# Kernel optimization log

Measured on AMD Instinct MI355X. Metric: run time of the kernel, lower is better.

The kernel has to match this reference:

```python
import jax, jax.numpy as jnp
import numpy as np

LN_EPS = 1e-5
ROPE_BASE = 10000.0


def rotate_half(x):
    # x: [..., d]; split into two halves (matches einops '(j d)->j d', j=2)
    d2 = x.shape[-1] // 2
    x1, x2 = x[..., :d2], x[..., d2:]
    return jnp.concatenate((-x2, x1), axis=-1)


def rotary_pos_emb(n, head_dim, dtype=jnp.float32):
    inv_freq = 1.0 / (ROPE_BASE ** (jnp.arange(0, head_dim, 2, dtype=jnp.float32) / head_dim))
    t = jnp.arange(n, dtype=jnp.float32)
    freqs = jnp.einsum('i,j->ij', t, inv_freq)          # [n, d/2]
    return jnp.concatenate((freqs, freqs), axis=-1).astype(dtype)  # [n, d]


def apply_rotary(pos, t):
    return t * jnp.cos(pos) + rotate_half(t) * jnp.sin(pos)


def setup_inputs() -> dict:
    key = jax.random.key(0)
    ks = jax.random.split(key, 4)
    b, n, dm = 2, 4096, 2048
    x = jax.random.normal(ks[0], (b, n, dm), dtype=jnp.float32)
    wq = jax.random.normal(ks[1], (dm, dm), dtype=jnp.float32) * (dm ** -0.5)
    wk = jax.random.normal(ks[2], (dm, dm), dtype=jnp.float32) * (dm ** -0.5)
    wv = jax.random.normal(ks[3], (dm, dm), dtype=jnp.float32) * (dm ** -0.5)
    return {
        'x': x,
        'ln_gamma': jnp.ones((dm,), jnp.float32),
        'ln_beta': jnp.zeros((dm,), jnp.float32),
        'wq': wq, 'wk': wk, 'wv': wv,
        'num_heads': 16,
    }


def reference(x, ln_gamma, ln_beta, wq, wk, wv, num_heads):
    b, n, dm = x.shape
    hd = dm // num_heads
    # LayerNorm (eps=1e-5, torch default)
    mu = jnp.mean(x, axis=-1, keepdims=True)
    var = jnp.mean(jnp.square(x - mu), axis=-1, keepdims=True)
    xn = (x - mu) * jax.lax.rsqrt(var + LN_EPS) * ln_gamma + ln_beta
    # QKV projections (nn.Linear, bias=False => x @ W.T; weights stored as [out,in])
    q = jnp.einsum('bnd,ed->bne', xn, wq)
    k = jnp.einsum('bnd,ed->bne', xn, wk)
    v = jnp.einsum('bnd,ed->bne', xn, wv)
    # b n (h d) -> b h n d
    split = lambda t: t.reshape(b, n, num_heads, hd).transpose(0, 2, 1, 3)
    q, k, v = split(q), split(k), split(v)
    pos = rotary_pos_emb(n, hd, x.dtype)  # [n, hd], broadcasts over b,h
    q = apply_rotary(pos, q)
    k = apply_rotary(pos, k)
    return q, k, v
```

## Files before the change

kernel.cpp:

```cpp
#include <hip/hip_runtime.h>
#include <hip/hip_bf16.h>


typedef float f32x4 __attribute__((ext_vector_type(4)));
typedef __bf16 bf16x8 __attribute__((ext_vector_type(8)));
typedef __bf16 bf16x4 __attribute__((ext_vector_type(4)));

#define DM    2048
#define NSEQ  4096
#define NH    16
#define HD    128
#define NROWS 8192
#define MAT_ELEMS (2ull*NH*NSEQ*HD)

typedef __attribute__((address_space(1))) const void GV;
typedef __attribute__((address_space(3))) void LV;
__device__ __forceinline__ void gload_lds16(const void* g, void* l) {
    __builtin_amdgcn_global_load_lds((GV*)g, (LV*)l, 16, 0, 0);
}

__global__ __launch_bounds__(256)
void ln_kernel(const float* __restrict__ x, const float* __restrict__ g,
               const float* __restrict__ be, __bf16* __restrict__ xnb) {
    int row = blockIdx.x;
    int tid = threadIdx.x;
    const float4* xr = (const float4*)(x + (size_t)row * DM);
    float4 v0 = xr[tid];
    float4 v1 = xr[tid + 256];
    float s  = v0.x + v0.y + v0.z + v0.w + v1.x + v1.y + v1.z + v1.w;
    float ss = v0.x*v0.x + v0.y*v0.y + v0.z*v0.z + v0.w*v0.w
             + v1.x*v1.x + v1.y*v1.y + v1.z*v1.z + v1.w*v1.w;
#pragma unroll
    for (int o = 32; o > 0; o >>= 1) {
        s  += __shfl_down(s, o);
        ss += __shfl_down(ss, o);
    }
    __shared__ float red[10];
    int wave = tid >> 6, lane = tid & 63;
    if (lane == 0) { red[wave] = s; red[4 + wave] = ss; }
    __syncthreads();
    if (tid == 0) {
        float S  = red[0] + red[1] + red[2] + red[3];
        float SS = red[4] + red[5] + red[6] + red[7];
        float mu  = S * (1.0f / DM);
        float var = SS * (1.0f / DM) - mu * mu;
        red[8] = mu;
        red[9] = rsqrtf(var + 1e-5f);
    }
    __syncthreads();
    float mu = red[8], rs = red[9];

    const float4* gp = (const float4*)g;
    const float4* bp = (const float4*)be;
    bf16x4* orow = (bf16x4*)(xnb + (size_t)row * DM);
    {
        float4 g0 = gp[tid], b0 = bp[tid];
        bf16x4 o;
        o[0] = (__bf16)((v0.x - mu) * rs * g0.x + b0.x);
        o[1] = (__bf16)((v0.y - mu) * rs * g0.y + b0.y);
        o[2] = (__bf16)((v0.z - mu) * rs * g0.z + b0.z);
        o[3] = (__bf16)((v0.w - mu) * rs * g0.w + b0.w);
        orow[tid] = o;
    }
    {
        float4 g1 = gp[tid + 256], b1 = bp[tid + 256];
        bf16x4 o;
        o[0] = (__bf16)((v1.x - mu) * rs * g1.x + b1.x);
        o[1] = (__bf16)((v1.y - mu) * rs * g1.y + b1.y);
        o[2] = (__bf16)((v1.z - mu) * rs * g1.z + b1.z);
        o[3] = (__bf16)((v1.w - mu) * rs * g1.w + b1.w);
        orow[tid + 256] = o;
    }
}

__global__ __launch_bounds__(256)
void cvt3_kernel(const float* __restrict__ a0, const float* __restrict__ a1,
                 const float* __restrict__ a2, __bf16* __restrict__ o) {
    int bid = blockIdx.x;
    const float* a = (bid < 2048) ? a0 : (bid < 4096) ? a1 : a2;
    size_t base = ((size_t)(bid & 2047) * 256 + threadIdx.x) * 8;
    float4 v0 = *(const float4*)(a + base);
    float4 v1 = *(const float4*)(a + base + 4);
    bf16x8 r;
    r[0] = (__bf16)v0.x; r[1] = (__bf16)v0.y; r[2] = (__bf16)v0.z; r[3] = (__bf16)v0.w;
    r[4] = (__bf16)v1.x; r[5] = (__bf16)v1.y; r[6] = (__bf16)v1.z; r[7] = (__bf16)v1.w;
    *(bf16x8*)(o + (size_t)(bid >> 11) * 4194304 + base) = r;
}


__device__ __forceinline__ void loadA4(bf16x8 (&a)[4][2], const __bf16* Sp,
                                       int base, int mb, int o0) {
#pragma unroll
    for (int mi = 0; mi < 4; mi++)
#pragma unroll
        for (int ks = 0; ks < 2; ks++)
            a[mi][ks] = *(const bf16x8*)(Sp + base + (mb + mi) * 1024 + (o0 ^ (ks * 32)));
}
__device__ __forceinline__ void loadB2(bf16x8 (&b)[2][2], const __bf16* Sp,
                                       int base, int cb, int o0) {
#pragma unroll
    for (int f = 0; f < 2; f++)
#pragma unroll
        for (int ks = 0; ks < 2; ks++)
            b[f][ks] = *(const bf16x8*)(Sp + base + (f * 16 + (cb >> 1) * 64) * 64 + (o0 ^ (ks * 32)));
}

template<int RB, int CB>
__device__ __forceinline__ void cluster(f32x4 (&acc)[8][4], bf16x8 (&a)[4][2],
                                        bf16x8 (&b)[2][2]) {
    __builtin_amdgcn_s_setprio(1);
#pragma unroll
    for (int mi = 0; mi < 4; mi++)
#pragma unroll
        for (int ni = 0; ni < 2; ni++)
#pragma unroll
            for (int ks = 0; ks < 2; ks++)
                acc[RB + mi][CB + ni] = __builtin_amdgcn_mfma_f32_16x16x32_bf16(
                    a[mi][ks], b[ni][ks], acc[RB + mi][CB + ni], 0, 0, 0);
    __builtin_amdgcn_s_setprio(0);
}

#define FENCE asm volatile("" ::: "memory")
#define BAR   do { FENCE; __builtin_amdgcn_s_barrier(); FENCE; } while (0)
#define VM8   asm volatile("s_waitcnt vmcnt(8)" ::: "memory")
#define VM4   asm volatile("s_waitcnt vmcnt(4)" ::: "memory")
#define VM2   asm volatile("s_waitcnt vmcnt(2)" ::: "memory")
#define VM0   asm volatile("s_waitcnt vmcnt(0)" ::: "memory")
#define VMX   do {} while (0)

#define STGA(P, kt, HF) do { \
    gload_lds16(pA + (size_t)((HF) * 64 + w * 8) * DM + (kt) * 64,       &As[P][((HF) * 8 + w) * 512]); \
    gload_lds16(pA + (size_t)((HF) * 64 + 128 + w * 8) * DM + (kt) * 64, &As[P][((HF) * 8 + 16 + w) * 512]); \
} while (0)
#define STGB(P, kt, HF) do { \
    gload_lds16(pB + (size_t)((HF) * 64 + w * 8) * DM + (kt) * 64,       &Bs[P][((HF) * 8 + w) * 512]); \
    gload_lds16(pB + (size_t)((HF) * 64 + 128 + w * 8) * DM + (kt) * 64, &Bs[P][((HF) * 8 + 16 + w) * 512]); \
} while (0)

#define KTILE(kt, P, Q, SG0, SG1, SG2, SG3, W0, W1, W2, W3) do { \
     \
    loadA4(a,  &As[P][0], baseA, 0, o0); \
    loadB2(b0, &Bs[P][0], baseB, 0, o0); \
    if (SG0) STGA(Q, (kt) + 1, 1);                \
    W0; BAR; cluster<0, 0>(acc, a, b0); BAR; \
     \
    loadB2(b1, &Bs[P][0], baseB, 2, o0); \
    if (SG1) STGA(P, (kt) + 2, 0);                \
    W1; BAR; cluster<0, 2>(acc, a, b1); BAR; \
     \
    loadA4(a, &As[P][0], baseA, 4, o0); \
    if (SG2) STGB(P, (kt) + 2, 0);                \
    W2; BAR; cluster<4, 2>(acc, a, b1); BAR; \
     \
    if (SG3) STGB(P, (kt) + 2, 1);                \
    W3; BAR; cluster<4, 0>(acc, a, b0); BAR; \
} while (0)

__global__ __launch_bounds__(512, 2)
void gemm_qkv(const __bf16* __restrict__ A,
              const __bf16* __restrict__ Wq,
              const __bf16* __restrict__ Wk,
              const __bf16* __restrict__ Wv,
              float* __restrict__ out) {
    __shared__ __bf16 As[2][16384];
    __shared__ __bf16 Bs[2][16384];

    int tid = threadIdx.x;
    int w = tid >> 6, l = tid & 63;
    int wm = w >> 2, wn = w & 3;

    int bid = blockIdx.x;
    int x = bid & 7;
    int ridx = bid >> 3;
    int q = ridx >> 5;
    int s = ridx & 31;
    int mtp, ntp;
    if (q == 0)      { mtp = s >> 3;       ntp = s & 7; }
    else if (q == 1) { mtp = 4 + (s >> 3); ntp = s & 7; }
    else             { mtp = s & 7;        ntp = 8 + (s >> 3); }
    int mt = (x & 3) * 8 + mtp;
    int nt = (x >> 2) * 12 + ntp;
    int mat = nt >> 3, ntb = nt & 7;
    const __bf16* Wp = (mat == 0) ? Wq : (mat == 1) ? Wk : Wv;
    int row0 = mt * 256, colp = ntb * 256;

    int lr = l >> 3;
    int lco = ((l & 7) ^ lr) * 8;
    const __bf16* pA = A  + (size_t)(row0 + lr) * DM + lco;
    const __bf16* pB = Wp + (size_t)(colp + lr) * DM + lco;

    int baseA = (wm * 128 + (l & 15)) * 64;
    int baseB = ((wn & 1) * 32 + (wn >> 1) * 128 + (l & 15)) * 64;
    int o0 = ((l >> 4) * 8) ^ ((l & 7) * 8);

    STGA(0, 0, 0); STGA(0, 0, 1); STGB(0, 0, 0); STGB(0, 0, 1);
    STGA(1, 1, 0); STGB(1, 1, 0); STGB(1, 1, 1);

    f32x4 acc[8][4];
#pragma unroll
    for (int i = 0; i < 8; i++)
#pragma unroll
        for (int j = 0; j < 4; j++)
            acc[i][j] = (f32x4){0.f, 0.f, 0.f, 0.f};

    bf16x8 a[4][2], b0[2][2], b1[2][2];

    VM8;
    BAR;

#pragma unroll 1
    for (int kt = 0; kt < 30; kt += 2) {
        KTILE(kt,     0, 1, 1, 1, 1, 1, VM8, VM8, VMX, VM8);
        KTILE(kt + 1, 1, 0, 1, 1, 1, 1, VM8, VM8, VMX, VM8);
    }
    KTILE(30, 0, 1, 1, 0, 0, 0, VM8, VM8, VMX, VM4);
    KTILE(31, 1, 0, 0, 0, 0, 0, VM2, VM0, VMX, VMX);

    float* op = out + (size_t)mat * MAT_ELEMS;
    int hd_lo = (wn & 1) * 32 + (l & 15);
    int head = ntb * 2 + (wn >> 1);
    int r_base = row0 + wm * 128 + ((l >> 4) << 2);
    float if0 = exp2f(-0.20762051f * (float)hd_lo);
    float if1 = exp2f(-0.20762051f * (float)(hd_lo + 16));

    if (mat < 2) {
#pragma unroll
        for (int mi = 0; mi < 8; mi++) {
#pragma unroll
            for (int j = 0; j < 4; j++) {
                int r = r_base + mi * 16 + j;
                int b = r >> 12, n = r & 4095;
                float fn = (float)n;
                float* rowp = op + ((size_t)((b * NH + head) * NSEQ + n)) * HD;
#pragma unroll
                for (int ni = 0; ni < 2; ni++) {
                    float lo = acc[mi][ni][j], hi = acc[mi][ni + 2][j];
                    float sv, cv;
                    __sincosf(fn * (ni ? if1 : if0), &sv, &cv);
                    rowp[hd_lo + ni * 16]      = lo * cv - hi * sv;
                    rowp[hd_lo + ni * 16 + 64] = hi * cv + lo * sv;
                }
            }
        }
    } else {
#pragma unroll
        for (int mi = 0; mi < 8; mi++) {
#pragma unroll
            for (int j = 0; j < 4; j++) {
                int r = r_base + mi * 16 + j;
                int b = r >> 12, n = r & 4095;
                float* rowp = op + ((size_t)((b * NH + head) * NSEQ + n)) * HD;
#pragma unroll
                for (int ni = 0; ni < 2; ni++) {
                    rowp[hd_lo + ni * 16]      = acc[mi][ni][j];
                    rowp[hd_lo + ni * 16 + 64] = acc[mi][ni + 2][j];
                }
            }
        }
    }
}

extern "C" void kernel_launch(void* const* d_in, const int* in_sizes, int n_in,
                              void* d_out, int out_size, void* d_ws, size_t ws_size,
                              hipStream_t stream) {
    const float* x  = (const float*)d_in[0];
    const float* g  = (const float*)d_in[1];
    const float* be = (const float*)d_in[2];
    const float* wq = (const float*)d_in[3];
    const float* wk = (const float*)d_in[4];
    const float* wv = (const float*)d_in[5];
    float* out = (float*)d_out;

    char* ws = (char*)d_ws;
    __bf16* xnb = (__bf16*)ws;
    __bf16* wb  = (__bf16*)(ws + 33554432);

    ln_kernel<<<NROWS, 256, 0, stream>>>(x, g, be, xnb);
    cvt3_kernel<<<6144, 256, 0, stream>>>(wq, wk, wv, wb);
    gemm_qkv<<<768, 512, 0, stream>>>(xnb, wb, wb + 4194304, wb + 8388608, out);
}
```

Measured before the change: 225.3 us.

## Restructure GEMM k-tile into k-split phases with full N fragments per cluster

Each 64-wide k-tile is now split into two 32-wide k halves. Each compute phase loads four A and four B fragments for one k half and issues 16 MFMAs over the full 4-column output, where before each phase covered two columns and both k halves. The global-to-LDS staging is regrouped so the A and B half-tiles for kt+2 are issued together, and the vmcnt wait points and the prologue load order change to match. The aim is to cut LDS fragment reloads (B is read once per k half instead of twice per tile) and rebalance memory waits, at the cost of more live fragment registers and a different overlap of loads with MFMA work.

```diff
diff --git a/kernel.cpp b/kernel.cpp
--- a/kernel.cpp
+++ b/kernel.cpp
@@ -88,42 +88,36 @@
 }
 
 
-__device__ __forceinline__ void loadA4(bf16x8 (&a)[4][2], const __bf16* Sp,
-                                       int base, int mb, int o0) {
+__device__ __forceinline__ void loadA(bf16x8 (&a)[4], const __bf16* Sp,
+                                      int base, int oo) {
 #pragma unroll
     for (int mi = 0; mi < 4; mi++)
-#pragma unroll
-        for (int ks = 0; ks < 2; ks++)
-            a[mi][ks] = *(const bf16x8*)(Sp + base + (mb + mi) * 1024 + (o0 ^ (ks * 32)));
-}
-__device__ __forceinline__ void loadB2(bf16x8 (&b)[2][2], const __bf16* Sp,
-                                       int base, int cb, int o0) {
-#pragma unroll
-    for (int f = 0; f < 2; f++)
-#pragma unroll
-        for (int ks = 0; ks < 2; ks++)
-            b[f][ks] = *(const bf16x8*)(Sp + base + (f * 16 + (cb >> 1) * 64) * 64 + (o0 ^ (ks * 32)));
-}
-
-template<int RB, int CB>
-__device__ __forceinline__ void cluster(f32x4 (&acc)[8][4], bf16x8 (&a)[4][2],
-                                        bf16x8 (&b)[2][2]) {
+        a[mi] = *(const bf16x8*)(Sp + base + mi * 1024 + oo);
+}
+__device__ __forceinline__ void loadB(bf16x8 (&b)[4], const __bf16* Sp,
+                                      int base, int oo) {
+#pragma unroll
+    for (int j = 0; j < 4; j++)
+        b[j] = *(const bf16x8*)(Sp + base + (j * 16 + (j >> 1) * 32) * 64 + oo);
+}
+
+template<int RB>
+__device__ __forceinline__ void cluster(f32x4 (&acc)[8][4], bf16x8 (&a)[4],
+                                        bf16x8 (&b)[4]) {
     __builtin_amdgcn_s_setprio(1);
 #pragma unroll
     for (int mi = 0; mi < 4; mi++)
 #pragma unroll
-        for (int ni = 0; ni < 2; ni++)
-#pragma unroll
-            for (int ks = 0; ks < 2; ks++)
-                acc[RB + mi][CB + ni] = __builtin_amdgcn_mfma_f32_16x16x32_bf16(
-                    a[mi][ks], b[ni][ks], acc[RB + mi][CB + ni], 0, 0, 0);
+        for (int ni = 0; ni < 4; ni++)
+            acc[RB + mi][ni] = __builtin_amdgcn_mfma_f32_16x16x32_bf16(
+                a[mi], b[ni], acc[RB + mi][ni], 0, 0, 0);
     __builtin_amdgcn_s_setprio(0);
 }
 
 #define FENCE asm volatile("" ::: "memory")
 #define BAR   do { FENCE; __builtin_amdgcn_s_barrier(); FENCE; } while (0)
 #define VM8   asm volatile("s_waitcnt vmcnt(8)" ::: "memory")
-#define VM4   asm volatile("s_waitcnt vmcnt(4)" ::: "memory")
+#define VM6   asm volatile("s_waitcnt vmcnt(6)" ::: "memory")
 #define VM2   asm volatile("s_waitcnt vmcnt(2)" ::: "memory")
 #define VM0   asm volatile("s_waitcnt vmcnt(0)" ::: "memory")
 #define VMX   do {} while (0)
@@ -137,23 +131,24 @@
     gload_lds16(pB + (size_t)((HF) * 64 + 128 + w * 8) * DM + (kt) * 64, &Bs[P][((HF) * 8 + 16 + w) * 512]); \
 } while (0)
 
-#define KTILE(kt, P, Q, SG0, SG1, SG2, SG3, W0, W1, W2, W3) do { \
-     \
-    loadA4(a,  &As[P][0], baseA, 0, o0); \
-    loadB2(b0, &Bs[P][0], baseB, 0, o0); \
-    if (SG0) STGA(Q, (kt) + 1, 1);                \
-    W0; BAR; cluster<0, 0>(acc, a, b0); BAR; \
-     \
-    loadB2(b1, &Bs[P][0], baseB, 2, o0); \
-    if (SG1) STGA(P, (kt) + 2, 0);                \
-    W1; BAR; cluster<0, 2>(acc, a, b1); BAR; \
-     \
-    loadA4(a, &As[P][0], baseA, 4, o0); \
-    if (SG2) STGB(P, (kt) + 2, 0);                \
-    W2; BAR; cluster<4, 2>(acc, a, b1); BAR; \
-     \
-    if (SG3) STGB(P, (kt) + 2, 1);                \
-    W3; BAR; cluster<4, 0>(acc, a, b0); BAR; \
+#define KTILE(kt, P, Q, SG0, SG2, SG3, W0, W2) do { \
+     \
+    loadA(a0, &As[P][0], baseA, o0); \
+    loadB(b0, &Bs[P][0], baseB, o0); \
+    if (SG0) STGA(Q, (kt) + 1, 1); \
+    W0; BAR; cluster<0>(acc, a0, b0); BAR; \
+     \
+    loadA(a1, &As[P][0], baseA, o1); \
+    loadB(b1, &Bs[P][0], baseB, o1); \
+    BAR; cluster<0>(acc, a1, b1); BAR; \
+     \
+    loadA(a0, &As[P][0], baseA + 4096, o0); \
+    if (SG2) { STGA(P, (kt) + 2, 0); STGB(P, (kt) + 2, 0); } \
+    W2; BAR; cluster<4>(acc, a0, b0); BAR; \
+     \
+    loadA(a1, &As[P][0], baseA + 4096, o1); \
+    if (SG3) STGB(P, (kt) + 2, 1); \
+    BAR; cluster<4>(acc, a1, b1); BAR; \
 } while (0)
 
 __global__ __launch_bounds__(512, 2)
@@ -192,8 +187,9 @@
     int baseA = (wm * 128 + (l & 15)) * 64;
     int baseB = ((wn & 1) * 32 + (wn >> 1) * 128 + (l & 15)) * 64;
     int o0 = ((l >> 4) * 8) ^ ((l & 7) * 8);
-
-    STGA(0, 0, 0); STGA(0, 0, 1); STGB(0, 0, 0); STGB(0, 0, 1);
+    int o1 = o0 ^ 32;
+
+    STGA(0, 0, 0); STGB(0, 0, 0); STGB(0, 0, 1); STGA(0, 0, 1);
     STGA(1, 1, 0); STGB(1, 1, 0); STGB(1, 1, 1);
 
     f32x4 acc[8][4];
@@ -203,18 +199,18 @@
         for (int j = 0; j < 4; j++)
             acc[i][j] = (f32x4){0.f, 0.f, 0.f, 0.f};
 
-    bf16x8 a[4][2], b0[2][2], b1[2][2];
+    bf16x8 a0[4], a1[4], b0[4], b1[4];
 
     VM8;
     BAR;
 
 #pragma unroll 1
     for (int kt = 0; kt < 30; kt += 2) {
-        KTILE(kt,     0, 1, 1, 1, 1, 1, VM8, VM8, VMX, VM8);
-        KTILE(kt + 1, 1, 0, 1, 1, 1, 1, VM8, VM8, VMX, VM8);
-    }
-    KTILE(30, 0, 1, 1, 0, 0, 0, VM8, VM8, VMX, VM4);
-    KTILE(31, 1, 0, 0, 0, 0, 0, VM2, VM0, VMX, VMX);
+        KTILE(kt,     0, 1, 1, 1, 1, VM8, VM6);
+        KTILE(kt + 1, 1, 0, 1, 1, 1, VM8, VM6);
+    }
+    KTILE(30, 0, 1, 1, 0, 0, VM8, VM2);
+    KTILE(31, 1, 0, 0, 0, 0, VM0, VMX);
 
     float* op = out + (size_t)mat * MAT_ELEMS;
     int hd_lo = (wn & 1) * 32 + (l & 15);
```

After: 233.8 us. 1.04x slower.

## Fuse LayerNorm and weight conversion launches; restructure GEMM vmcnt/lgkm waits

Applied to the files above, without the earlier changes.

Merges the LayerNorm and fp32-to-bf16 weight conversion kernels into one launch that branches on block index, removing one kernel launch and its tail. In the GEMM main loop the per-stage vmcnt waits are replaced by a single vmcnt(6) wait per k-tile plus an explicit lgkmcnt(0) wait and scheduling barrier after each barrier. The prologue load order is also changed to match. This may cut wait stalls but risks serializing LDS reads before the MFMA clusters.

```diff
diff --git a/kernel.cpp b/kernel.cpp
--- a/kernel.cpp
+++ b/kernel.cpp
@@ -20,71 +20,73 @@
 }
 
 __global__ __launch_bounds__(256)
-void ln_kernel(const float* __restrict__ x, const float* __restrict__ g,
-               const float* __restrict__ be, __bf16* __restrict__ xnb) {
-    int row = blockIdx.x;
+void lncvt_kernel(const float* __restrict__ x, const float* __restrict__ g,
+                  const float* __restrict__ be,
+                  const float* __restrict__ wq, const float* __restrict__ wk,
+                  const float* __restrict__ wv,
+                  __bf16* __restrict__ xnb, __bf16* __restrict__ wb) {
+    int bid = blockIdx.x;
     int tid = threadIdx.x;
-    const float4* xr = (const float4*)(x + (size_t)row * DM);
-    float4 v0 = xr[tid];
-    float4 v1 = xr[tid + 256];
-    float s  = v0.x + v0.y + v0.z + v0.w + v1.x + v1.y + v1.z + v1.w;
-    float ss = v0.x*v0.x + v0.y*v0.y + v0.z*v0.z + v0.w*v0.w
-             + v1.x*v1.x + v1.y*v1.y + v1.z*v1.z + v1.w*v1.w;
-#pragma unroll
-    for (int o = 32; o > 0; o >>= 1) {
-        s  += __shfl_down(s, o);
-        ss += __shfl_down(ss, o);
+    if (bid < NROWS) {
+        int row = bid;
+        const float4* xr = (const float4*)(x + (size_t)row * DM);
+        float4 v0 = xr[tid];
+        float4 v1 = xr[tid + 256];
+        float s  = v0.x + v0.y + v0.z + v0.w + v1.x + v1.y + v1.z + v1.w;
+        float ss = v0.x*v0.x + v0.y*v0.y + v0.z*v0.z + v0.w*v0.w
+                 + v1.x*v1.x + v1.y*v1.y + v1.z*v1.z + v1.w*v1.w;
+#pragma unroll
+        for (int o = 32; o > 0; o >>= 1) {
+            s  += __shfl_down(s, o);
+            ss += __shfl_down(ss, o);
+        }
+        __shared__ float red[10];
+        int wave = tid >> 6, lane = tid & 63;
+        if (lane == 0) { red[wave] = s; red[4 + wave] = ss; }
+        __syncthreads();
+        if (tid == 0) {
+            float S  = red[0] + red[1] + red[2] + red[3];
+            float SS = red[4] + red[5] + red[6] + red[7];
+            float mu  = S * (1.0f / DM);
+            float var = SS * (1.0f / DM) - mu * mu;
+            red[8] = mu;
+            red[9] = rsqrtf(var + 1e-5f);
+        }
+        __syncthreads();
+        float mu = red[8], rs = red[9];
+
+        const float4* gp = (const float4*)g;
+        const float4* bp = (const float4*)be;
+        bf16x4* orow = (bf16x4*)(xnb + (size_t)row * DM);
+        {
+            float4 g0 = gp[tid], b0 = bp[tid];
+            bf16x4 o;
+            o[0] = (__bf16)((v0.x - mu) * rs * g0.x + b0.x);
+            o[1] = (__bf16)((v0.y - mu) * rs * g0.y + b0.y);
+            o[2] = (__bf16)((v0.z - mu) * rs * g0.z + b0.z);
+            o[3] = (__bf16)((v0.w - mu) * rs * g0.w + b0.w);
+            orow[tid] = o;
+        }
+        {
+            float4 g1 = gp[tid + 256], b1 = bp[tid + 256];
+            bf16x4 o;
+            o[0] = (__bf16)((v1.x - mu) * rs * g1.x + b1.x);
+            o[1] = (__bf16)((v1.y - mu) * rs * g1.y + b1.y);
+            o[2] = (__bf16)((v1.z - mu) * rs * g1.z + b1.z);
+            o[3] = (__bf16)((v1.w - mu) * rs * g1.w + b1.w);
+            orow[tid + 256] = o;
+        }
+    } else {
+        int cb = bid - NROWS;
+        const float* a = (cb < 2048) ? wq : (cb < 4096) ? wk : wv;
+        size_t base = ((size_t)(cb & 2047) * 256 + tid) * 8;
+        float4 v0 = *(const float4*)(a + base);
+        float4 v1 = *(const float4*)(a + base + 4);
+        bf16x8 r;
+        r[0] = (__bf16)v0.x; r[1] = (__bf16)v0.y; r[2] = (__bf16)v0.z; r[3] = (__bf16)v0.w;
+        r[4] = (__bf16)v1.x; r[5] = (__bf16)v1.y; r[6] = (__bf16)v1.z; r[7] = (__bf16)v1.w;
+        *(bf16x8*)(wb + (size_t)(cb >> 11) * 4194304 + base) = r;
     }
-    __shared__ float red[10];
-    int wave = tid >> 6, lane = tid & 63;
-    if (lane == 0) { red[wave] = s; red[4 + wave] = ss; }
-    __syncthreads();
-    if (tid == 0) {
-        float S  = red[0] + red[1] + red[2] + red[3];
-        float SS = red[4] + red[5] + red[6] + red[7];
-        float mu  = S * (1.0f / DM);
-        float var = SS * (1.0f / DM) - mu * mu;
-        red[8] = mu;
-        red[9] = rsqrtf(var + 1e-5f);
-    }
-    __syncthreads();
-    float mu = red[8], rs = red[9];
-
-    const float4* gp = (const float4*)g;
-    const float4* bp = (const float4*)be;
-    bf16x4* orow = (bf16x4*)(xnb + (size_t)row * DM);
-    {
-        float4 g0 = gp[tid], b0 = bp[tid];
-        bf16x4 o;
-        o[0] = (__bf16)((v0.x - mu) * rs * g0.x + b0.x);
-        o[1] = (__bf16)((v0.y - mu) * rs * g0.y + b0.y);
-        o[2] = (__bf16)((v0.z - mu) * rs * g0.z + b0.z);
-        o[3] = (__bf16)((v0.w - mu) * rs * g0.w + b0.w);
-        orow[tid] = o;
-    }
-    {
-        float4 g1 = gp[tid + 256], b1 = bp[tid + 256];
-        bf16x4 o;
-        o[0] = (__bf16)((v1.x - mu) * rs * g1.x + b1.x);
-        o[1] = (__bf16)((v1.y - mu) * rs * g1.y + b1.y);
-        o[2] = (__bf16)((v1.z - mu) * rs * g1.z + b1.z);
-        o[3] = (__bf16)((v1.w - mu) * rs * g1.w + b1.w);
-        orow[tid + 256] = o;
-    }
-}
-
-__global__ __launch_bounds__(256)
-void cvt3_kernel(const float* __restrict__ a0, const float* __restrict__ a1,
-                 const float* __restrict__ a2, __bf16* __restrict__ o) {
-    int bid = blockIdx.x;
-    const float* a = (bid < 2048) ? a0 : (bid < 4096) ? a1 : a2;
-    size_t base = ((size_t)(bid & 2047) * 256 + threadIdx.x) * 8;
-    float4 v0 = *(const float4*)(a + base);
-    float4 v1 = *(const float4*)(a + base + 4);
-    bf16x8 r;
-    r[0] = (__bf16)v0.x; r[1] = (__bf16)v0.y; r[2] = (__bf16)v0.z; r[3] = (__bf16)v0.w;
-    r[4] = (__bf16)v1.x; r[5] = (__bf16)v1.y; r[6] = (__bf16)v1.z; r[7] = (__bf16)v1.w;
-    *(bf16x8*)(o + (size_t)(bid >> 11) * 4194304 + base) = r;
 }
 
 
@@ -122,9 +124,9 @@
 
 #define FENCE asm volatile("" ::: "memory")
 #define BAR   do { FENCE; __builtin_amdgcn_s_barrier(); FENCE; } while (0)
-#define VM8   asm volatile("s_waitcnt vmcnt(8)" ::: "memory")
-#define VM4   asm volatile("s_waitcnt vmcnt(4)" ::: "memory")
-#define VM2   asm volatile("s_waitcnt vmcnt(2)" ::: "memory")
+#define BARO  do { BAR; asm volatile("s_waitcnt lgkmcnt(0)" ::: "memory"); \
+                   __builtin_amdgcn_sched_barrier(0); } while (0)
+#define VM6   asm volatile("s_waitcnt vmcnt(6)" ::: "memory")
 #define VM0   asm volatile("s_waitcnt vmcnt(0)" ::: "memory")
 #define VMX   do {} while (0)
 
@@ -137,23 +139,24 @@
     gload_lds16(pB + (size_t)((HF) * 64 + 128 + w * 8) * DM + (kt) * 64, &Bs[P][((HF) * 8 + 16 + w) * 512]); \
 } while (0)
 
-#define KTILE(kt, P, Q, SG0, SG1, SG2, SG3, W0, W1, W2, W3) do { \
+#define KTILE(kt, P, Q, SG0, SG1, SG2, SG3, W3) do { \
      \
     loadA4(a,  &As[P][0], baseA, 0, o0); \
     loadB2(b0, &Bs[P][0], baseB, 0, o0); \
     if (SG0) STGA(Q, (kt) + 1, 1);                \
-    W0; BAR; cluster<0, 0>(acc, a, b0); BAR; \
+    BARO; cluster<0, 0>(acc, a, b0); BAR; \
      \
     loadB2(b1, &Bs[P][0], baseB, 2, o0); \
     if (SG1) STGA(P, (kt) + 2, 0);                \
-    W1; BAR; cluster<0, 2>(acc, a, b1); BAR; \
+    BARO; cluster<0, 2>(acc, a, b1); BAR; \
      \
     loadA4(a, &As[P][0], baseA, 4, o0); \
     if (SG2) STGB(P, (kt) + 2, 0);                \
-    W2; BAR; cluster<4, 2>(acc, a, b1); BAR; \
+    BARO; cluster<4, 2>(acc, a, b1); BAR; \
      \
     if (SG3) STGB(P, (kt) + 2, 1);                \
-    W3; BAR; cluster<4, 0>(acc, a, b0); BAR; \
+    W3; \
+    BARO; cluster<4, 0>(acc, a, b0); BAR; \
 } while (0)
 
 __global__ __launch_bounds__(512, 2)
@@ -193,7 +196,7 @@
     int baseB = ((wn & 1) * 32 + (wn >> 1) * 128 + (l & 15)) * 64;
     int o0 = ((l >> 4) * 8) ^ ((l & 7) * 8);
 
-    STGA(0, 0, 0); STGA(0, 0, 1); STGB(0, 0, 0); STGB(0, 0, 1);
+    STGA(0, 0, 0); STGB(0, 0, 0); STGB(0, 0, 1); STGA(0, 0, 1);
     STGA(1, 1, 0); STGB(1, 1, 0); STGB(1, 1, 1);
 
     f32x4 acc[8][4];
@@ -205,16 +208,16 @@
 
     bf16x8 a[4][2], b0[2][2], b1[2][2];
 
-    VM8;
+    VM6;
     BAR;
 
 #pragma unroll 1
     for (int kt = 0; kt < 30; kt += 2) {
-        KTILE(kt,     0, 1, 1, 1, 1, 1, VM8, VM8, VMX, VM8);
-        KTILE(kt + 1, 1, 0, 1, 1, 1, 1, VM8, VM8, VMX, VM8);
+        KTILE(kt,     0, 1, 1, 1, 1, 1, VM6);
+        KTILE(kt + 1, 1, 0, 1, 1, 1, 1, VM6);
     }
-    KTILE(30, 0, 1, 1, 0, 0, 0, VM8, VM8, VMX, VM4);
-    KTILE(31, 1, 0, 0, 0, 0, 0, VM2, VM0, VMX, VMX);
+    KTILE(30, 0, 1, 1, 0, 0, 0, VM0);
+    KTILE(31, 1, 0, 0, 0, 0, 0, VMX);
 
     float* op = out + (size_t)mat * MAT_ELEMS;
     int hd_lo = (wn & 1) * 32 + (l & 15);
@@ -275,7 +278,6 @@
     __bf16* xnb = (__bf16*)ws;
     __bf16* wb  = (__bf16*)(ws + 33554432);
 
-    ln_kernel<<<NROWS, 256, 0, stream>>>(x, g, be, xnb);
-    cvt3_kernel<<<6144, 256, 0, stream>>>(wq, wk, wv, wb);
+    lncvt_kernel<<<NROWS + 6144, 256, 0, stream>>>(x, g, be, wq, wk, wv, xnb, wb);
     gemm_qkv<<<768, 512, 0, stream>>>(xnb, wb, wb + 4194304, wb + 8388608, out);
 }
```

Result: no change. 221.5 us (median of 2 runs) (-1.7%).
